# Kernel optimization log

Hardware: AMD Instinct MI355X
Metric: run time of the kernel (lower is better)

Reference implementation:

```python
import jax, jax.numpy as jnp
import numpy as np

NODE_DIM = 256
EDGE_H = 128
B, N = 2, 512
EPS = 1e-5

def _layernorm(x, g, b):
    mu = jnp.mean(x, axis=-1, keepdims=True)
    var = jnp.mean((x - mu) ** 2, axis=-1, keepdims=True)
    return (x - mu) * jax.lax.rsqrt(var + EPS) * g + b

def setup_inputs() -> dict:
    key = jax.random.key(0)
    ks = jax.random.split(key, 12)
    s = lambda k, shape, fan: jax.random.normal(k, shape, jnp.float32) * (1.0 / np.sqrt(fan))
    return {
        "latent_values": jax.random.normal(ks[0], (B, N, NODE_DIM), jnp.float32),
        "sn_g": jnp.ones((NODE_DIM,), jnp.float32),
        "sn_b": jnp.zeros((NODE_DIM,), jnp.float32),
        "tn_g": jnp.ones((NODE_DIM,), jnp.float32),
        "tn_b": jnp.zeros((NODE_DIM,), jnp.float32),
        "sW": s(ks[1], (EDGE_H, NODE_DIM), NODE_DIM),
        "sb": jnp.zeros((EDGE_H,), jnp.float32),
        "tW": s(ks[2], (EDGE_H, NODE_DIM), NODE_DIM),
        "tb": jnp.zeros((EDGE_H,), jnp.float32),
        "W1": s(ks[3], (EDGE_H, 3 * EDGE_H), 3 * EDGE_H),
        "b1": jnp.zeros((EDGE_H,), jnp.float32),
        "W2": s(ks[4], (1, EDGE_H), EDGE_H),
        "b2": jnp.zeros((1,), jnp.float32),
    }

def reference(latent_values, sn_g, sn_b, tn_g, tn_b, sW, sb, tW, tb, W1, b1, W2, b2):
    # projected source/target features: [B, N, H]
    src = _layernorm(latent_values, sn_g, sn_b) @ sW.T + sb
    tgt = _layernorm(latent_values, tn_g, tn_b) @ tW.T + tb
    # first MLP linear on concat([src_i, tgt_j, src_i*tgt_j]) decomposed into
    # three H-blocks of W1 -- same math, no 3H concat materialized.
    Ws, Wt, Wp = W1[:, :EDGE_H], W1[:, EDGE_H:2 * EDGE_H], W1[:, 2 * EDGE_H:]
    h = (src @ Ws.T)[:, :, None, :] + (tgt @ Wt.T)[:, None, :, :]
    h = h + jnp.einsum("bih,bjh,kh->bijk", src, tgt, Wp) + b1  # [B, N, N, H]
    h = jax.nn.gelu(h, approximate=False)
    logits = jnp.einsum("bijk,k->bij", h, W2[0]) + b2[0]
    edges = logits / (1.0 + jnp.abs(logits))  # softsign
    # mask self-edges (allow_self_edges=False)
    diag = jnp.eye(N, dtype=bool)
    return jnp.where(diag[None, :, :], 0.0, edges)
```

## Files before the change

kernel.cpp:

```cpp
#include <hip/hip_runtime.h>
#include <math.h>

#define BN 512
#define ND 256
#define EH 128

typedef __attribute__((ext_vector_type(8))) short short8v;
typedef __attribute__((ext_vector_type(4))) float f32x4;

__device__ __forceinline__ unsigned short f2bf_rn(float x) {
  unsigned int u = __float_as_uint(x);
  unsigned int r = u + 0x7FFFu + ((u >> 16) & 1u);
  return (unsigned short)(r >> 16);
}
__device__ __forceinline__ float bf2f(unsigned short h) {
  return __uint_as_float(((unsigned int)h) << 16);
}

__global__ __launch_bounds__(256) void prep_kernel(
    const float* __restrict__ latent,
    const float* __restrict__ sng, const float* __restrict__ snb,
    const float* __restrict__ tng, const float* __restrict__ tnb,
    const float* __restrict__ sW,  const float* __restrict__ sb,
    const float* __restrict__ tW,  const float* __restrict__ tbv,
    const float* __restrict__ W1,  const float* __restrict__ b1,
    float* __restrict__ srcg, float* __restrict__ apreg,
    unsigned short* __restrict__ tgtb)
{
  __shared__ float lns[4][256];
  __shared__ float lnt[4][256];
  __shared__ float ssrc[4][128];
  const int tid = threadIdx.x;
  const int w = tid >> 6, lane = tid & 63;
  const int row0 = blockIdx.x << 2;

  {
    const int row = row0 + w;
    const float* x = latent + (size_t)row * ND;
    const int h = lane << 2;
    float4 xv = *(const float4*)(x + h);
    float s1 = xv.x + xv.y + xv.z + xv.w;
    float s2 = xv.x*xv.x + xv.y*xv.y + xv.z*xv.z + xv.w*xv.w;
    #pragma unroll
    for (int m = 1; m < 64; m <<= 1) {
      s1 += __shfl_xor(s1, m, 64);
      s2 += __shfl_xor(s2, m, 64);
    }
    const float mu  = s1 * (1.0f/256.0f);
    const float var = s2 * (1.0f/256.0f) - mu*mu;
    const float rstd = rsqrtf(var + 1e-5f);
    float4 ga = *(const float4*)(sng + h), ba = *(const float4*)(snb + h);
    float4 gb = *(const float4*)(tng + h), bb = *(const float4*)(tnb + h);
    const float n0 = (xv.x - mu)*rstd, n1 = (xv.y - mu)*rstd;
    const float n2 = (xv.z - mu)*rstd, n3 = (xv.w - mu)*rstd;
    lns[w][h+0] = n0*ga.x + ba.x; lns[w][h+1] = n1*ga.y + ba.y;
    lns[w][h+2] = n2*ga.z + ba.z; lns[w][h+3] = n3*ga.w + ba.w;
    lnt[w][h+0] = n0*gb.x + bb.x; lnt[w][h+1] = n1*gb.y + bb.y;
    lnt[w][h+2] = n2*gb.z + bb.z; lnt[w][h+3] = n3*gb.w + bb.w;
  }
  __syncthreads();

  const int side = tid >> 7, k = tid & 127;
  {
    const float* W = side ? tW : sW;
    const float bias = side ? tbv[k] : sb[k];
    const float (*L)[256] = side ? lnt : lns;
    float a0 = bias, a1 = bias, a2 = bias, a3 = bias;
    const float* wr = W + (size_t)k * ND;
    for (int h4 = 0; h4 < ND; h4 += 4) {
      float4 wv = *(const float4*)(wr + h4);
      float4 l0 = *(const float4*)&L[0][h4];
      float4 l1 = *(const float4*)&L[1][h4];
      float4 l2 = *(const float4*)&L[2][h4];
      float4 l3 = *(const float4*)&L[3][h4];
      a0 += wv.x*l0.x + wv.y*l0.y + wv.z*l0.z + wv.w*l0.w;
      a1 += wv.x*l1.x + wv.y*l1.y + wv.z*l1.z + wv.w*l1.w;
      a2 += wv.x*l2.x + wv.y*l2.y + wv.z*l2.z + wv.w*l2.w;
      a3 += wv.x*l3.x + wv.y*l3.y + wv.z*l3.z + wv.w*l3.w;
    }
    if (!side) {
      ssrc[0][k]=a0; ssrc[1][k]=a1; ssrc[2][k]=a2; ssrc[3][k]=a3;
      srcg[(size_t)(row0+0)*EH+k]=a0; srcg[(size_t)(row0+1)*EH+k]=a1;
      srcg[(size_t)(row0+2)*EH+k]=a2; srcg[(size_t)(row0+3)*EH+k]=a3;
    } else {
      tgtb[(size_t)(row0+0)*EH + k] = f2bf_rn(a0);
      tgtb[(size_t)(row0+1)*EH + k] = f2bf_rn(a1);
      tgtb[(size_t)(row0+2)*EH + k] = f2bf_rn(a2);
      tgtb[(size_t)(row0+3)*EH + k] = f2bf_rn(a3);
    }
  }
  __syncthreads();

  {
    const int kk = tid & 127, half = tid >> 7;
    const float bb = b1[kk];
    float a0 = bb, a1 = bb;
    const float* wr = W1 + (size_t)kk * 384;
    const int r0 = half * 2;
    for (int h4 = 0; h4 < EH; h4 += 4) {
      float4 wv = *(const float4*)(wr + h4);
      float4 l0 = *(const float4*)&ssrc[r0][h4];
      float4 l1 = *(const float4*)&ssrc[r0+1][h4];
      a0 += wv.x*l0.x + wv.y*l0.y + wv.z*l0.z + wv.w*l0.w;
      a1 += wv.x*l1.x + wv.y*l1.y + wv.z*l1.z + wv.w*l1.w;
    }
    apreg[(size_t)(row0+r0)*EH + kk]   = a0;
    apreg[(size_t)(row0+r0+1)*EH + kk] = a1;
  }
}

__global__ __launch_bounds__(256, 2) void edge_kernel(
    const float* __restrict__ srcg, const float* __restrict__ apreg,
    const unsigned short* __restrict__ tgtb,
    const float* __restrict__ W1, const float* __restrict__ W2,
    const float* __restrict__ b2, float* __restrict__ out)
{
  __shared__ __align__(16) unsigned short Gs[128 * 128];
  __shared__ float s_src[128];

  const int tid = threadIdx.x;
  const int l = tid & 63, w = tid >> 6;
  const int blk = blockIdx.x;
  const int b = blk >> 9, i = blk & 511;

  if (tid < 128) s_src[tid] = srcg[(size_t)blk * EH + tid];
  __syncthreads();

  {
    const int k = tid >> 1, h0 = (tid & 1) * 64;
    const float* wpr = W1 + (size_t)k * 384 + 256 + h0;
    const float* wtr = W1 + (size_t)k * 384 + 128 + h0;
    const unsigned int swz = (unsigned int)((k & 15) << 4);
    char* gB = (char*)Gs + k * 256;
    #pragma unroll
    for (int c = 0; c < 64; c += 8) {
      float4 wpa = *(const float4*)(wpr + c);
      float4 wpb = *(const float4*)(wpr + c + 4);
      float4 wta = *(const float4*)(wtr + c);
      float4 wtb = *(const float4*)(wtr + c + 4);
      float4 sa  = *(const float4*)&s_src[h0 + c];
      float4 sb4 = *(const float4*)&s_src[h0 + c + 4];
      short8v hv;
      hv[0] = (short)f2bf_rn(fmaf(sa.x,  wpa.x, wta.x));
      hv[1] = (short)f2bf_rn(fmaf(sa.y,  wpa.y, wta.y));
      hv[2] = (short)f2bf_rn(fmaf(sa.z,  wpa.z, wta.z));
      hv[3] = (short)f2bf_rn(fmaf(sa.w,  wpa.w, wta.w));
      hv[4] = (short)f2bf_rn(fmaf(sb4.x, wpb.x, wtb.x));
      hv[5] = (short)f2bf_rn(fmaf(sb4.y, wpb.y, wtb.y));
      hv[6] = (short)f2bf_rn(fmaf(sb4.z, wpb.z, wtb.z));
      hv[7] = (short)f2bf_rn(fmaf(sb4.w, wpb.w, wtb.w));
      const unsigned int off = ((unsigned int)((h0 + c) * 2)) ^ swz;
      *(short8v*)(gB + off) = hv;
    }
  }
  __syncthreads();

  const int l15 = l & 15;
  const int hi4 = l >> 4;
  float apv[8], w2v[8];
  #pragma unroll
  for (int nt = 0; nt < 8; ++nt) {
    apv[nt] = apreg[(size_t)blk * EH + nt * 16 + l15];
    w2v[nt] = W2[nt * 16 + l15];
  }
  const float b2s = b2[0];

  const unsigned short* tB = tgtb + (size_t)b * BN * EH;
  float* orow = out + (size_t)blk * BN;

  const int cb = hi4 * 16;
  const unsigned int swzl = (unsigned int)(l15 << 4);

#define LOADA(buf, ks_)                                                        \
  {                                                                            \
    _Pragma("unroll")                                                          \
    for (int m = 0; m < 4; ++m) {                                              \
      const size_t r = (size_t)(jt0 + m * 16 + l15) * EH + (ks_) * 32 + hi4 * 8;\
      buf[m] = *(const short8v*)(tB + r);                                      \
    }                                                                          \
  }

#define MFMA_STEP(buf, ks_)                                                    \
  {                                                                            \
    _Pragma("unroll")                                                          \
    for (int nt = 0; nt < 8; ++nt) {                                           \
      const int rowoff = nt * 4096 + l15 * 256;                                \
      const unsigned int col = ((unsigned int)(((ks_) << 6) | cb)) ^ swzl;     \
      short8v bfr = *(const short8v*)((const char*)Gs + rowoff + col);         \
      _Pragma("unroll")                                                        \
      for (int m = 0; m < 4; ++m)                                              \
        acc[m][nt] = __builtin_amdgcn_mfma_f32_16x16x32_bf16(buf[m], bfr, acc[m][nt], 0, 0, 0); \
    }                                                                          \
  }

  #pragma unroll 1
  for (int p = 0; p < 2; ++p) {
    const int jt0 = (w * 8 + p * 4) * 16;
    f32x4 acc[4][8];
    #pragma unroll
    for (int m = 0; m < 4; ++m)
      #pragma unroll
      for (int nt = 0; nt < 8; ++nt)
        acc[m][nt] = (f32x4){apv[nt], apv[nt], apv[nt], apv[nt]};

    short8v aA[4], aB[4];
    LOADA(aA, 0)
    #pragma unroll 1
    for (int kk = 0; kk < 2; ++kk) {
      const int ks0 = kk * 2;
      LOADA(aB, ks0 + 1)
      MFMA_STEP(aA, ks0)
      if (kk == 0) LOADA(aA, 2)
      MFMA_STEP(aB, ks0 + 1)
    }

    #pragma unroll
    for (int m = 0; m < 4; ++m) {
      float ov[4];
      #pragma unroll
      for (int reg = 0; reg < 4; ++reg) {
        float ps = 0.0f;
        #pragma unroll
        for (int nt = 0; nt < 8; ++nt) {
          const float x  = acc[m][nt][reg];
          const float x2 = x * x;
          const float q = fmaf(x2, -0.10294817f, -2.3022077f);
          const float e = __builtin_amdgcn_exp2f(x * q);
          const float r = __builtin_amdgcn_rcpf(1.0f + e);
          ps = fmaf(w2v[nt], x * r, ps);
        }
        ps += __shfl_xor(ps, 1, 64);
        ps += __shfl_xor(ps, 2, 64);
        ps += __shfl_xor(ps, 4, 64);
        ps += __shfl_xor(ps, 8, 64);
        const float s = ps + b2s;
        ov[reg] = s / (1.0f + fabsf(s));
      }
      if (l15 == 0) {
        const int j0 = jt0 + m * 16 + hi4 * 4;
        float4 o4 = {(j0 + 0 == i) ? 0.0f : ov[0],
                     (j0 + 1 == i) ? 0.0f : ov[1],
                     (j0 + 2 == i) ? 0.0f : ov[2],
                     (j0 + 3 == i) ? 0.0f : ov[3]};
        *(float4*)(orow + j0) = o4;
      }
    }
  }
#undef LOADA
#undef MFMA_STEP
}

extern "C" void kernel_launch(void* const* d_in, const int* in_sizes, int n_in,
                              void* d_out, int out_size, void* d_ws, size_t ws_size,
                              hipStream_t stream) {
  const float* latent = (const float*)d_in[0];
  const float* sng = (const float*)d_in[1];
  const float* snb = (const float*)d_in[2];
  const float* tng = (const float*)d_in[3];
  const float* tnb = (const float*)d_in[4];
  const float* sW  = (const float*)d_in[5];
  const float* sb  = (const float*)d_in[6];
  const float* tW  = (const float*)d_in[7];
  const float* tb  = (const float*)d_in[8];
  const float* W1  = (const float*)d_in[9];
  const float* b1  = (const float*)d_in[10];
  const float* W2  = (const float*)d_in[11];
  const float* b2  = (const float*)d_in[12];
  float* out = (float*)d_out;

  float* ws = (float*)d_ws;
  float* srcg  = ws;
  float* apreg = ws + 131072;
  unsigned short* tgtb = (unsigned short*)(ws + 262144);

  hipLaunchKernelGGL(prep_kernel, dim3(256), dim3(256), 0, stream,
                     latent, sng, snb, tng, tnb, sW, sb, tW, tb, W1, b1,
                     srcg, apreg, tgtb);
  hipLaunchKernelGGL(edge_kernel, dim3(1024), dim3(256), 0, stream,
                     srcg, apreg, tgtb, W1, W2, b2, out);
}
```

Baseline: 68.93 us.

## Swap MFMA operand roles, prefetch target tiles early, pack GELU epilogue math

In the edge kernel, the MFMA operands are swapped so the hidden dimension lies along the accumulator rows. The per-j reduction then becomes an in-register sum plus two cross-lane shuffles instead of four. The first target-feature loads are issued before the G-table build, and the next pass's loads are software-pipelined across passes to hide global latency. The GELU epilogue uses packed float2 math with apre and W2 staged in shared memory, and the prep-kernel dot loops get unroll pragmas. The trade-offs are more live registers under the 2-blocks-per-SM bound and a different output store pattern, one float per lane instead of a float4.

```diff
diff --git a/kernel.cpp b/kernel.cpp
--- a/kernel.cpp
+++ b/kernel.cpp
@@ -7,6 +7,7 @@
 
 typedef __attribute__((ext_vector_type(8))) short short8v;
 typedef __attribute__((ext_vector_type(4))) float f32x4;
+typedef __attribute__((ext_vector_type(2))) float f32x2;
 
 __device__ __forceinline__ unsigned short f2bf_rn(float x) {
   unsigned int u = __float_as_uint(x);
@@ -67,6 +68,7 @@
     const float (*L)[256] = side ? lnt : lns;
     float a0 = bias, a1 = bias, a2 = bias, a3 = bias;
     const float* wr = W + (size_t)k * ND;
+    #pragma unroll 4
     for (int h4 = 0; h4 < ND; h4 += 4) {
       float4 wv = *(const float4*)(wr + h4);
       float4 l0 = *(const float4*)&L[0][h4];
@@ -97,6 +99,7 @@
     float a0 = bb, a1 = bb;
     const float* wr = W1 + (size_t)kk * 384;
     const int r0 = half * 2;
+    #pragma unroll 4
     for (int h4 = 0; h4 < EH; h4 += 4) {
       float4 wv = *(const float4*)(wr + h4);
       float4 l0 = *(const float4*)&ssrc[r0][h4];
@@ -117,14 +120,39 @@
 {
   __shared__ __align__(16) unsigned short Gs[128 * 128];
   __shared__ float s_src[128];
+  __shared__ __align__(16) float s_apre[128];
+  __shared__ __align__(16) float s_w2[128];
 
   const int tid = threadIdx.x;
   const int l = tid & 63, w = tid >> 6;
   const int blk = blockIdx.x;
   const int b = blk >> 9, i = blk & 511;
 
-  if (tid < 128) s_src[tid] = srcg[(size_t)blk * EH + tid];
-  __syncthreads();
+  if (tid < 128) {
+    s_src[tid]  = srcg[(size_t)blk * EH + tid];
+    s_apre[tid] = apreg[(size_t)blk * EH + tid];
+    s_w2[tid]   = W2[tid];
+  }
+  __syncthreads();
+
+  const int l15 = l & 15;
+  const int hi4 = l >> 4;
+  const unsigned short* tB = tgtb + (size_t)b * BN * EH;
+  float* orow = out + (size_t)blk * BN;
+  const float b2s = b2[0];
+
+#define LOADB(buf, jtb_, ks_)                                                  \
+  {                                                                            \
+    _Pragma("unroll")                                                          \
+    for (int q_ = 0; q_ < 4; ++q_) {                                           \
+      const size_t r_ = (size_t)((jtb_) + q_ * 16 + l15) * EH + (ks_) * 32 + hi4 * 8; \
+      buf[q_] = *(const short8v*)(tB + r_);                                    \
+    }                                                                          \
+  }
+
+  short8v bufA[4], bufB[4];
+  LOADB(bufA, w * 128, 0)
+  LOADB(bufB, w * 128, 1)
 
   {
     const int k = tid >> 1, h0 = (tid & 1) * 64;
@@ -155,99 +183,88 @@
   }
   __syncthreads();
 
-  const int l15 = l & 15;
-  const int hi4 = l >> 4;
-  float apv[8], w2v[8];
-  #pragma unroll
-  for (int nt = 0; nt < 8; ++nt) {
-    apv[nt] = apreg[(size_t)blk * EH + nt * 16 + l15];
-    w2v[nt] = W2[nt * 16 + l15];
-  }
-  const float b2s = b2[0];
-
-  const unsigned short* tB = tgtb + (size_t)b * BN * EH;
-  float* orow = out + (size_t)blk * BN;
-
   const int cb = hi4 * 16;
   const unsigned int swzl = (unsigned int)(l15 << 4);
-
-#define LOADA(buf, ks_)                                                        \
-  {                                                                            \
-    _Pragma("unroll")                                                          \
-    for (int m = 0; m < 4; ++m) {                                              \
-      const size_t r = (size_t)(jt0 + m * 16 + l15) * EH + (ks_) * 32 + hi4 * 8;\
-      buf[m] = *(const short8v*)(tB + r);                                      \
-    }                                                                          \
-  }
 
 #define MFMA_STEP(buf, ks_)                                                    \
   {                                                                            \
     _Pragma("unroll")                                                          \
-    for (int nt = 0; nt < 8; ++nt) {                                           \
-      const int rowoff = nt * 4096 + l15 * 256;                                \
+    for (int mt = 0; mt < 8; ++mt) {                                           \
+      const int rowoff = mt * 4096 + l15 * 256;                                \
       const unsigned int col = ((unsigned int)(((ks_) << 6) | cb)) ^ swzl;     \
-      short8v bfr = *(const short8v*)((const char*)Gs + rowoff + col);         \
+      short8v afr = *(const short8v*)((const char*)Gs + rowoff + col);         \
       _Pragma("unroll")                                                        \
-      for (int m = 0; m < 4; ++m)                                              \
-        acc[m][nt] = __builtin_amdgcn_mfma_f32_16x16x32_bf16(buf[m], bfr, acc[m][nt], 0, 0, 0); \
+      for (int q_ = 0; q_ < 4; ++q_)                                           \
+        acc[q_][mt] = __builtin_amdgcn_mfma_f32_16x16x32_bf16(afr, buf[q_], acc[q_][mt], 0, 0, 0); \
     }                                                                          \
+  }
+
+#define GELU_PK(xp, wp)                                                        \
+  {                                                                            \
+    const f32x2 x2_ = (xp) * (xp);                                             \
+    const f32x2 qv_ = x2_ * (-0.10294817f) + (f32x2){-2.3022077f, -2.3022077f};\
+    const f32x2 tv_ = (xp) * qv_;                                              \
+    const f32x2 ev_ = (f32x2){__builtin_amdgcn_exp2f(tv_[0]),                  \
+                              __builtin_amdgcn_exp2f(tv_[1])};                 \
+    const f32x2 dv_ = ev_ + 1.0f;                                              \
+    const f32x2 rv_ = (f32x2){__builtin_amdgcn_rcpf(dv_[0]),                   \
+                              __builtin_amdgcn_rcpf(dv_[1])};                  \
+    ps += (wp) * ((xp) * rv_);                                                 \
   }
 
   #pragma unroll 1
   for (int p = 0; p < 2; ++p) {
-    const int jt0 = (w * 8 + p * 4) * 16;
+    const int jtb  = w * 128 + p * 64;
+    const int jtbN = w * 128 + ((p + 1) & 1) * 64;
     f32x4 acc[4][8];
     #pragma unroll
-    for (int m = 0; m < 4; ++m)
+    for (int mt = 0; mt < 8; ++mt) {
+      const f32x4 apm = *(const f32x4*)&s_apre[mt * 16 + hi4 * 4];
       #pragma unroll
-      for (int nt = 0; nt < 8; ++nt)
-        acc[m][nt] = (f32x4){apv[nt], apv[nt], apv[nt], apv[nt]};
-
-    short8v aA[4], aB[4];
-    LOADA(aA, 0)
-    #pragma unroll 1
-    for (int kk = 0; kk < 2; ++kk) {
-      const int ks0 = kk * 2;
-      LOADA(aB, ks0 + 1)
-      MFMA_STEP(aA, ks0)
-      if (kk == 0) LOADA(aA, 2)
-      MFMA_STEP(aB, ks0 + 1)
-    }
-
-    #pragma unroll
-    for (int m = 0; m < 4; ++m) {
-      float ov[4];
+      for (int q = 0; q < 4; ++q) acc[q][mt] = apm;
+    }
+
+    MFMA_STEP(bufA, 0)
+    LOADB(bufA, jtb, 2)
+    MFMA_STEP(bufB, 1)
+    LOADB(bufB, jtb, 3)
+    MFMA_STEP(bufA, 2)
+    LOADB(bufA, jtbN, 0)
+    MFMA_STEP(bufB, 3)
+    LOADB(bufB, jtbN, 1)
+
+    #pragma unroll
+    for (int q = 0; q < 4; ++q) {
+      f32x2 ps = (f32x2){0.0f, 0.0f};
       #pragma unroll
-      for (int reg = 0; reg < 4; ++reg) {
-        float ps = 0.0f;
-        #pragma unroll
-        for (int nt = 0; nt < 8; ++nt) {
-          const float x  = acc[m][nt][reg];
-          const float x2 = x * x;
-          const float q = fmaf(x2, -0.10294817f, -2.3022077f);
-          const float e = __builtin_amdgcn_exp2f(x * q);
-          const float r = __builtin_amdgcn_rcpf(1.0f + e);
-          ps = fmaf(w2v[nt], x * r, ps);
+      for (int mt = 0; mt < 8; ++mt) {
+        const f32x4 x4 = acc[q][mt];
+        const f32x4 w4 = *(const f32x4*)&s_w2[mt * 16 + hi4 * 4];
+        {
+          const f32x2 xp = __builtin_shufflevector(x4, x4, 0, 1);
+          const f32x2 wp = __builtin_shufflevector(w4, w4, 0, 1);
+          GELU_PK(xp, wp)
         }
-        ps += __shfl_xor(ps, 1, 64);
-        ps += __shfl_xor(ps, 2, 64);
-        ps += __shfl_xor(ps, 4, 64);
-        ps += __shfl_xor(ps, 8, 64);
-        const float s = ps + b2s;
-        ov[reg] = s / (1.0f + fabsf(s));
+        {
+          const f32x2 xp = __builtin_shufflevector(x4, x4, 2, 3);
+          const f32x2 wp = __builtin_shufflevector(w4, w4, 2, 3);
+          GELU_PK(xp, wp)
+        }
       }
-      if (l15 == 0) {
-        const int j0 = jt0 + m * 16 + hi4 * 4;
-        float4 o4 = {(j0 + 0 == i) ? 0.0f : ov[0],
-                     (j0 + 1 == i) ? 0.0f : ov[1],
-                     (j0 + 2 == i) ? 0.0f : ov[2],
-                     (j0 + 3 == i) ? 0.0f : ov[3]};
-        *(float4*)(orow + j0) = o4;
+      float pstot = ps[0] + ps[1];
+      pstot += __shfl_xor(pstot, 16, 64);
+      pstot += __shfl_xor(pstot, 32, 64);
+      const float s = pstot + b2s;
+      const float e2 = s / (1.0f + fabsf(s));
+      if (hi4 == 0) {
+        const int j = jtb + q * 16 + l15;
+        orow[j] = (j == i) ? 0.0f : e2;
       }
     }
   }
-#undef LOADA
+#undef LOADB
 #undef MFMA_STEP
+#undef GELU_PK
 }
 
 extern "C" void kernel_launch(void* const* d_in, const int* in_sizes, int n_in,
```

Result: slower. 141.4 us (+105.2%).
